# Performance work log

Measured on AMD Instinct MI355X. Metric: run time of the kernel, lower is better.

The kernel has to match this reference:

```python
import jax, jax.numpy as jnp
import numpy as np

N = 65536   # number of input points
M = 4096    # subsample_size (centroids)
K = 64      # group_limit (neighborhood size)
RADIUS = 0.2  # group_radius


def _mlp(x, W1, b1, W2, b2, W3, b3):
    # PyG MLP([6, 64, 64, 128], act='relu'); batch_norm with default running
    # stats (mean 0, var 1) is identity, so: Linear-ReLU-Linear-ReLU-Linear.
    h = jax.nn.relu(x @ W1 + b1)
    h = jax.nn.relu(h @ W2 + b2)
    return h @ W3 + b3


def setup_inputs() -> dict:
    key = jax.random.key(0)
    ks = jax.random.split(key, 8)
    vertices = jax.random.normal(ks[0], (N, 3), dtype=jnp.float32)
    centroid_indices = jax.random.randint(ks[1], (M,), 0, N)

    def lin(k, fi, fo):
        return (jax.random.normal(k, (fi, fo), dtype=jnp.float32) / np.sqrt(fi)).astype(jnp.float32)

    return {
        "vertices": vertices,
        "centroid_indices": centroid_indices,
        "W1": lin(ks[2], 6, 64),  "b1": jnp.zeros((64,), jnp.float32),
        "W2": lin(ks[3], 64, 64), "b2": jnp.zeros((64,), jnp.float32),
        "W3": lin(ks[4], 64, 128), "b3": jnp.zeros((128,), jnp.float32),
    }


def reference(vertices, centroid_indices, W1, b1, W2, b2, W3, b3):
    # --- group_around_centroids ---
    sq_norm = jnp.einsum('ij,ij->i', vertices, vertices)          # [N]
    cpos = vertices[centroid_indices]                              # [M,3]
    # faithful distance formula: sqrt(|sn_c - 2 c.v + sn|)
    d = jnp.sqrt(jnp.abs(sq_norm[centroid_indices][:, None]
                         - 2.0 * (cpos @ vertices.T)
                         + sq_norm[None, :]))                      # [M,N]  (~1 GB)
    # K nearest per centroid (equivalent to masking by k-th sorted distance)
    neg_dk, idx = jax.lax.top_k(-d, K)                             # [M,K]
    d_k = -neg_dk                                                  # ascending distances
    limit = jnp.minimum(d_k[:, K - 1], RADIUS)                     # [M]
    mask = d_k <= limit[:, None]                                   # [M,K]

    # --- PointNetConv: msg = MLP(cat[x_j, pos_j - pos_i]), max-aggregate to centroid ---
    pos_j = vertices[idx]                                          # [M,K,3]
    feat = jnp.concatenate([pos_j, pos_j - cpos[:, None, :]], axis=-1)  # [M,K,6]
    h = _mlp(feat, W1, b1, W2, b2, W3, b3)                         # [M,K,128]
    h = jnp.where(mask[:, :, None], h, -jnp.inf)
    return jnp.max(h, axis=1)                                      # [M,128]
```

## Files before the change

### kernel.cpp

```cpp
#include <hip/hip_runtime.h>
#include <hip/hip_bf16.h>

#define GD     50
#define NC     (GD*GD*GD)
#define CAPK   256
#define RADIUS_F 0.2f
#define R2SAFE 0.0401f

typedef unsigned long long ull;
typedef __attribute__((ext_vector_type(4))) _Float16 f16x4;
typedef __attribute__((ext_vector_type(8))) _Float16 f16x8;
typedef __attribute__((ext_vector_type(4))) float    f32x4;

__device__ __forceinline__ int cellcoord(float v) {
    int c = (int)floorf((v + 5.0f) * 5.0f);
    return min(max(c, 0), GD - 1);
}

__global__ void sa_zero_kernel(int4* __restrict__ dst, int n4) {
    int i = blockIdx.x * blockDim.x + threadIdx.x;
    int stride = gridDim.x * blockDim.x;
    for (; i < n4; i += stride) dst[i] = make_int4(0, 0, 0, 0);
}

__global__ void sa_prep_kernel(const float* __restrict__ vtx,
                               float4* __restrict__ pt4,
                               int* __restrict__ cid,
                               int* __restrict__ cellCnt,
                               int N,
                               const float* __restrict__ W1,
                               const float* __restrict__ W2,
                               const float* __restrict__ W3,
                               _Float16* __restrict__ wf16) {
    int i = blockIdx.x * blockDim.x + threadIdx.x;
    int stride = gridDim.x * blockDim.x;
    for (int p = i; p < N; p += stride) {
        float x = vtx[3 * p], y = vtx[3 * p + 1], z = vtx[3 * p + 2];
        float sn = fmaf(z, z, fmaf(y, y, x * x));
        pt4[p] = make_float4(x, y, z, sn);
        int cc = (cellcoord(z) * GD + cellcoord(y)) * GD + cellcoord(x);
        cid[p] = cc;
        atomicAdd(&cellCnt[cc], 1);
    }
    for (int e = i; e < 1024; e += stride) {
        int col = e >> 4, k = e & 15;
        wf16[e] = (k < 6) ? (_Float16)W1[k * 64 + col] : (_Float16)0.f;
    }
    for (int e = i; e < 4096; e += stride) {
        int col = e >> 6, k = e & 63;
        wf16[1024 + e] = (_Float16)W2[k * 64 + col];
    }
    for (int e = i; e < 8192; e += stride) {
        int col = e >> 6, k = e & 63;
        wf16[5120 + e] = (_Float16)W3[k * 128 + col];
    }
}

__global__ __launch_bounds__(256) void sa_offsets_kernel(
    const int* __restrict__ cellCnt, int* __restrict__ cellStart,
    int* __restrict__ cellCur, int* __restrict__ cursor) {
    __shared__ int sc[256];
    __shared__ int base_s;
    int t = threadIdx.x;
    int i = blockIdx.x * 256 + t;
    int c = (i < NC) ? cellCnt[i] : 0;
    sc[t] = c;
    __syncthreads();
    for (int d = 1; d < 256; d <<= 1) {
        int o = (t >= d) ? sc[t - d] : 0;
        __syncthreads();
        sc[t] += o;
        __syncthreads();
    }
    if (t == 255) base_s = atomicAdd(cursor, sc[255]);
    __syncthreads();
    int start = base_s + sc[t] - c;
    if (i < NC) { cellStart[i] = start; cellCur[i] = start; }
}

__global__ void sa_scatter_kernel(const float4* __restrict__ pt4,
                                  const int* __restrict__ cid,
                                  int* __restrict__ cellCur,
                                  float4* __restrict__ sorted4,
                                  int* __restrict__ sidx, int N) {
    int p = blockIdx.x * blockDim.x + threadIdx.x;
    if (p < N) {
        int pos = atomicAdd(&cellCur[cid[p]], 1);
        sorted4[pos] = pt4[p];
        sidx[pos] = p;
    }
}

__global__ __launch_bounds__(256) void sa_collect_kernel(
    const float4* __restrict__ pt4, const int* __restrict__ cidx,
    const float4* __restrict__ sorted4, const int* __restrict__ sidx,
    const int* __restrict__ cellCnt, const int* __restrict__ cellStart,
    _Float16* __restrict__ featG, int* __restrict__ nselG) {

    __shared__ ull keys[4][CAPK];
    __shared__ int selb[4][64];
    __shared__ int scnt_s[4];

    int t = threadIdx.x, w = t >> 6, lane = t & 63;
    int c = blockIdx.x * 4 + w;
    float4 cc = pt4[cidx[c]];

    int cx = cellcoord(cc.x), cy = cellcoord(cc.y), cz = cellcoord(cc.z);
    int x0 = max(cx - 1, 0), x1 = min(cx + 1, GD - 1), lx = x1 - x0 + 1;
    int y0 = max(cy - 1, 0), y1 = min(cy + 1, GD - 1), ly = y1 - y0 + 1;
    int z0 = max(cz - 1, 0), z1 = min(cz + 1, GD - 1), lz = z1 - z0 + 1;
    int L = lx * ly * lz;

    int cellc = 0, cstart = 0;
    if (lane < L) {
        int lxy = lx * ly;
        int iz = lane / lxy, rem = lane - iz * lxy;
        int iy = rem / lx, ix = rem - iy * lx;
        int gx = x0 + ix, gy = y0 + iy, gz = z0 + iz;
        float xlo = (gx == 0) ? -1e30f : gx * 0.2f - 5.0f;
        float xhi = (gx == GD - 1) ? 1e30f : (gx + 1) * 0.2f - 5.0f;
        float ylo = (gy == 0) ? -1e30f : gy * 0.2f - 5.0f;
        float yhi = (gy == GD - 1) ? 1e30f : (gy + 1) * 0.2f - 5.0f;
        float zlo = (gz == 0) ? -1e30f : gz * 0.2f - 5.0f;
        float zhi = (gz == GD - 1) ? 1e30f : (gz + 1) * 0.2f - 5.0f;
        float dx = fmaxf(0.f, fmaxf(xlo - cc.x, cc.x - xhi));
        float dy = fmaxf(0.f, fmaxf(ylo - cc.y, cc.y - yhi));
        float dz = fmaxf(0.f, fmaxf(zlo - cc.z, cc.z - zhi));
        if (fmaf(dz, dz, fmaf(dy, dy, dx * dx)) <= R2SAFE) {
            int cell = (gz * GD + gy) * GD + gx;
            cellc = cellCnt[cell];
            cstart = cellStart[cell];
        }
    }
    int pfx = cellc;
#pragma unroll
    for (int d = 1; d < 32; d <<= 1) {
        int o = __shfl_up(pfx, d);
        if (lane >= d) pfx += o;
    }
    int excl = pfx - cellc;
    if (lane == 0) scnt_s[w] = 0;
    int T = __shfl(pfx, L - 1);

    ull* key = keys[w];
    for (int base = 0; base < T; base += 64) {
        int s = base + lane;
        int lo = 0, hi = L - 1;
#pragma unroll 5
        for (int it = 0; it < 5; ++it) {
            int mid = (lo + hi + 1) >> 1;
            int em = __shfl(excl, mid);
            if (lo < hi) { if (em <= s) lo = mid; else hi = mid - 1; }
        }
        int sp = __shfl(cstart, lo) + (s - __shfl(excl, lo));
        if (s < T) {
            float4 p = sorted4[sp];
            float dot = fmaf(p.z, cc.z, fmaf(p.y, cc.y, p.x * cc.x));
            float tt = fmaf(-2.f, dot, cc.w) + p.w;
            if (tt <= R2SAFE) {
                float d = sqrtf(fabsf(tt));
                if (d <= RADIUS_F) {
                    int pid = sidx[sp];
                    int slot = atomicAdd(&scnt_s[w], 1);
                    if (slot < CAPK)
                        key[slot] = (((ull)__float_as_uint(d)) << 32) | (unsigned)pid;
                }
            }
        }
    }

    int n = min(scnt_s[w], CAPK);
    int nsel = min(n, 64);
    if (n > 64) {
        for (int i = lane; i < n; i += 64) {
            ull ki = key[i];
            int r = 0;
            for (int j = 0; j < n; ++j) r += (key[j] < ki) ? 1 : 0;
            if (r < 64) selb[w][r] = (int)(unsigned)(ki & 0xffffffffu);
        }
    } else {
        for (int i = lane; i < n; i += 64)
            selb[w][i] = (int)(unsigned)(key[i] & 0xffffffffu);
    }

    {
        _Float16 z = (_Float16)0.f;
        f16x8 lo8 = {z, z, z, z, z, z, z, z};
        if (lane < nsel) {
            float4 p = pt4[selb[w][lane]];
            lo8[0] = (_Float16)p.x; lo8[1] = (_Float16)p.y; lo8[2] = (_Float16)p.z;
            lo8[3] = (_Float16)(p.x - cc.x);
            lo8[4] = (_Float16)(p.y - cc.y);
            lo8[5] = (_Float16)(p.z - cc.z);
        }
        f16x8 hi8 = {z, z, z, z, z, z, z, z};
        _Float16* fr = featG + (size_t)c * 1024 + lane * 16;
        *(f16x8*)(fr + 0) = lo8;
        *(f16x8*)(fr + 8) = hi8;
    }
    if (lane == 0) nselG[c] = nsel;
}

__global__ __launch_bounds__(256) void sa_mlp2_kernel(
    const _Float16* __restrict__ featG, const int* __restrict__ nselG,
    const _Float16* __restrict__ wf16,
    const float* __restrict__ b1, const float* __restrict__ b2,
    const float* __restrict__ b3, float* __restrict__ out) {

    __shared__ __align__(16) _Float16 hbuf[4][4096];

    int t = threadIdx.x, w = t >> 6, lane = t & 63;
    int c = blockIdx.x * 4 + w;
    int nsel = nselG[c];

    int r16 = lane & 15, g = lane >> 4;
    _Float16* h = hbuf[w];
    const _Float16* fG = featG + (size_t)c * 1024;
    const _Float16* w1 = wf16;
    const _Float16* w2 = wf16 + 1024;
    const _Float16* w3 = wf16 + 5120;

    {
        f16x4 a1[4];
#pragma unroll
        for (int m = 0; m < 4; ++m)
            a1[m] = *(const f16x4*)&fG[(m * 16 + r16) * 16 + g * 4];
#pragma unroll
        for (int nn = 0; nn < 4; ++nn) {
            int col = nn * 16 + r16;
            f16x4 b = *(const f16x4*)&w1[col * 16 + g * 4];
            float bb = b1[col];
#pragma unroll
            for (int m = 0; m < 4; ++m) {
                f32x4 acc = {bb, bb, bb, bb};
                acc = __builtin_amdgcn_mfma_f32_16x16x16f16(a1[m], b, acc, 0, 0, 0);
#pragma unroll
                for (int reg = 0; reg < 4; ++reg) {
                    int row = m * 16 + g * 4 + reg;
                    h[row * 64 + (col ^ ((row & 7) << 3))] =
                        (_Float16)fmaxf(acc[reg], 0.f);
                }
            }
        }
    }

    {
        f16x8 a2[4][2];
#pragma unroll
        for (int m = 0; m < 4; ++m)
#pragma unroll
            for (int kt = 0; kt < 2; ++kt) {
                int row = m * 16 + r16;
                int k0 = kt * 32 + g * 8;
                a2[m][kt] = *(const f16x8*)&h[row * 64 + (k0 ^ ((row & 7) << 3))];
            }
#pragma unroll
        for (int nn = 0; nn < 4; ++nn) {
            int col = nn * 16 + r16;
            f16x8 bA = *(const f16x8*)&w2[col * 64 + g * 8];
            f16x8 bB = *(const f16x8*)&w2[col * 64 + 32 + g * 8];
            float bb = b2[col];
#pragma unroll
            for (int m = 0; m < 4; ++m) {
                f32x4 acc = {bb, bb, bb, bb};
                acc = __builtin_amdgcn_mfma_f32_16x16x32_f16(a2[m][0], bA, acc, 0, 0, 0);
                acc = __builtin_amdgcn_mfma_f32_16x16x32_f16(a2[m][1], bB, acc, 0, 0, 0);
#pragma unroll
                for (int reg = 0; reg < 4; ++reg) {
                    int row = m * 16 + g * 4 + reg;
                    h[row * 64 + (col ^ ((row & 7) << 3))] =
                        (_Float16)fmaxf(acc[reg], 0.f);
                }
            }
        }
    }

    {
        f16x8 a3[4][2];
#pragma unroll
        for (int m = 0; m < 4; ++m)
#pragma unroll
            for (int kt = 0; kt < 2; ++kt) {
                int row = m * 16 + r16;
                int k0 = kt * 32 + g * 8;
                a3[m][kt] = *(const f16x8*)&h[row * 64 + (k0 ^ ((row & 7) << 3))];
            }
        float ninf = __int_as_float(0xff800000);
#pragma unroll
        for (int nn = 0; nn < 8; ++nn) {
            int col = nn * 16 + r16;
            f16x8 bA = *(const f16x8*)&w3[col * 64 + g * 8];
            f16x8 bB = *(const f16x8*)&w3[col * 64 + 32 + g * 8];
            float bb = b3[col];
            float vm = ninf;
#pragma unroll
            for (int m = 0; m < 4; ++m) {
                f32x4 acc = {bb, bb, bb, bb};
                acc = __builtin_amdgcn_mfma_f32_16x16x32_f16(a3[m][0], bA, acc, 0, 0, 0);
                acc = __builtin_amdgcn_mfma_f32_16x16x32_f16(a3[m][1], bB, acc, 0, 0, 0);
#pragma unroll
                for (int reg = 0; reg < 4; ++reg) {
                    int row = m * 16 + g * 4 + reg;
                    if (row < nsel) vm = fmaxf(vm, acc[reg]);
                }
            }
            vm = fmaxf(vm, __shfl_xor(vm, 16));
            vm = fmaxf(vm, __shfl_xor(vm, 32));
            if (lane < 16) out[(size_t)c * 128 + nn * 16 + lane] = vm;
        }
    }
}

extern "C" void kernel_launch(void* const* d_in, const int* in_sizes, int n_in,
                              void* d_out, int out_size, void* d_ws, size_t ws_size,
                              hipStream_t stream) {
    const float* vtx = (const float*)d_in[0];
    const int* cidx  = (const int*)d_in[1];
    const float* W1  = (const float*)d_in[2];
    const float* b1  = (const float*)d_in[3];
    const float* W2  = (const float*)d_in[4];
    const float* b2  = (const float*)d_in[5];
    const float* W3  = (const float*)d_in[6];
    const float* b3  = (const float*)d_in[7];
    float* out = (float*)d_out;

    int N = in_sizes[0] / 3;
    int M = in_sizes[1];

    char* ws = (char*)d_ws;
    size_t off = 0;
    float4* pt4     = (float4*)(ws + off); off += (size_t)N * 16;
    float4* sorted4 = (float4*)(ws + off); off += (size_t)N * 16;
    int* sidx       = (int*)(ws + off);    off += (size_t)N * 4;
    int* cid        = (int*)(ws + off);    off += (size_t)N * 4;
    int* cellCnt    = (int*)(ws + off);    off += (size_t)NC * 4;
    int* cursor     = (int*)(ws + off);    off += 16;
    int* cellStart  = (int*)(ws + off);    off += (size_t)NC * 4;
    int* cellCur    = (int*)(ws + off);    off += (size_t)NC * 4;
    _Float16* featG = (_Float16*)(ws + off); off += (size_t)M * 1024 * 2;
    int* nselG      = (int*)(ws + off);    off += (size_t)M * 4;
    _Float16* wf16  = (_Float16*)(ws + off);

    sa_zero_kernel<<<256, 256, 0, stream>>>((int4*)cellCnt, (NC * 4 + 16) / 16);
    sa_prep_kernel<<<512, 256, 0, stream>>>(vtx, pt4, cid, cellCnt, N,
                                            W1, W2, W3, wf16);
    sa_offsets_kernel<<<(NC + 255) / 256, 256, 0, stream>>>(cellCnt, cellStart,
                                                            cellCur, cursor);
    sa_scatter_kernel<<<(N + 255) / 256, 256, 0, stream>>>(pt4, cid, cellCur,
                                                           sorted4, sidx, N);
    sa_collect_kernel<<<M / 4, 256, 0, stream>>>(pt4, cidx, sorted4, sidx,
                                                 cellCnt, cellStart, featG, nselG);
    sa_mlp2_kernel<<<M / 4, 256, 0, stream>>>(featG, nselG, wf16,
                                              b1, b2, b3, out);
}
```

Measured before the change: 72.71 us.

## Fuse neighbor collection and MLP kernels through shared memory

Merges the collect kernel and the MLP kernel into one, keeping each centroid's gathered features in per-wave LDS instead of writing them to a global workspace and reading them back. The key buffer and the hidden-activation buffer share one LDS region, with the feature tile placed in the upper half. This removes one launch and the global round trip of the feature tensor. In exchange the fused kernel uses more registers and LDS per block, which may lower occupancy, and correctness depends on the aliased LDS regions not overlapping while still live.

```diff
diff --git a/kernel.cpp b/kernel.cpp
--- a/kernel.cpp
+++ b/kernel.cpp
@@ -91,19 +91,25 @@
     }
 }
 
-__global__ __launch_bounds__(256) void sa_collect_kernel(
+__global__ __launch_bounds__(256) void sa_fused2_kernel(
     const float4* __restrict__ pt4, const int* __restrict__ cidx,
     const float4* __restrict__ sorted4, const int* __restrict__ sidx,
     const int* __restrict__ cellCnt, const int* __restrict__ cellStart,
-    _Float16* __restrict__ featG, int* __restrict__ nselG) {
-
-    __shared__ ull keys[4][CAPK];
+    const _Float16* __restrict__ wf16,
+    const float* __restrict__ b1, const float* __restrict__ b2,
+    const float* __restrict__ b3, float* __restrict__ out) {
+
+    __shared__ __align__(16) char smem[4][8192];
     __shared__ int selb[4][64];
     __shared__ int scnt_s[4];
 
     int t = threadIdx.x, w = t >> 6, lane = t & 63;
     int c = blockIdx.x * 4 + w;
     float4 cc = pt4[cidx[c]];
+
+    ull* key = (ull*)smem[w];
+    _Float16* featb = (_Float16*)(smem[w] + 4096);
+    _Float16* h = (_Float16*)smem[w];
 
     int cx = cellcoord(cc.x), cy = cellcoord(cc.y), cz = cellcoord(cc.z);
     int x0 = max(cx - 1, 0), x1 = min(cx + 1, GD - 1), lx = x1 - x0 + 1;
@@ -142,7 +148,6 @@
     if (lane == 0) scnt_s[w] = 0;
     int T = __shfl(pfx, L - 1);
 
-    ull* key = keys[w];
     for (int base = 0; base < T; base += 64) {
         int s = base + lane;
         int lo = 0, hi = L - 1;
@@ -194,28 +199,11 @@
             lo8[5] = (_Float16)(p.z - cc.z);
         }
         f16x8 hi8 = {z, z, z, z, z, z, z, z};
-        _Float16* fr = featG + (size_t)c * 1024 + lane * 16;
-        *(f16x8*)(fr + 0) = lo8;
-        *(f16x8*)(fr + 8) = hi8;
-    }
-    if (lane == 0) nselG[c] = nsel;
-}
-
-__global__ __launch_bounds__(256) void sa_mlp2_kernel(
-    const _Float16* __restrict__ featG, const int* __restrict__ nselG,
-    const _Float16* __restrict__ wf16,
-    const float* __restrict__ b1, const float* __restrict__ b2,
-    const float* __restrict__ b3, float* __restrict__ out) {
-
-    __shared__ __align__(16) _Float16 hbuf[4][4096];
-
-    int t = threadIdx.x, w = t >> 6, lane = t & 63;
-    int c = blockIdx.x * 4 + w;
-    int nsel = nselG[c];
+        *(f16x8*)&featb[lane * 16 + 0] = lo8;
+        *(f16x8*)&featb[lane * 16 + 8] = hi8;
+    }
 
     int r16 = lane & 15, g = lane >> 4;
-    _Float16* h = hbuf[w];
-    const _Float16* fG = featG + (size_t)c * 1024;
     const _Float16* w1 = wf16;
     const _Float16* w2 = wf16 + 1024;
     const _Float16* w3 = wf16 + 5120;
@@ -224,7 +212,7 @@
         f16x4 a1[4];
 #pragma unroll
         for (int m = 0; m < 4; ++m)
-            a1[m] = *(const f16x4*)&fG[(m * 16 + r16) * 16 + g * 4];
+            a1[m] = *(const f16x4*)&featb[(m * 16 + r16) * 16 + g * 4];
 #pragma unroll
         for (int nn = 0; nn < 4; ++nn) {
             int col = nn * 16 + r16;
@@ -337,8 +325,6 @@
     int* cursor     = (int*)(ws + off);    off += 16;
     int* cellStart  = (int*)(ws + off);    off += (size_t)NC * 4;
     int* cellCur    = (int*)(ws + off);    off += (size_t)NC * 4;
-    _Float16* featG = (_Float16*)(ws + off); off += (size_t)M * 1024 * 2;
-    int* nselG      = (int*)(ws + off);    off += (size_t)M * 4;
     _Float16* wf16  = (_Float16*)(ws + off);
 
     sa_zero_kernel<<<256, 256, 0, stream>>>((int4*)cellCnt, (NC * 4 + 16) / 16);
@@ -348,8 +334,7 @@
                                                             cellCur, cursor);
     sa_scatter_kernel<<<(N + 255) / 256, 256, 0, stream>>>(pt4, cid, cellCur,
                                                            sorted4, sidx, N);
-    sa_collect_kernel<<<M / 4, 256, 0, stream>>>(pt4, cidx, sorted4, sidx,
-                                                 cellCnt, cellStart, featG, nselG);
-    sa_mlp2_kernel<<<M / 4, 256, 0, stream>>>(featG, nselG, wf16,
-                                              b1, b2, b3, out);
-}
+    sa_fused2_kernel<<<M / 4, 256, 0, stream>>>(pt4, cidx, sorted4, sidx,
+                                                cellCnt, cellStart, wf16,
+                                                b1, b2, b3, out);
+}
```

Result: no change. 72.85 us (+0.2%).
